# Optimization experiments

Hardware: AMD Instinct MI355X
Metric: run time of the kernel (lower is better)

## Reference

```python
import jax, jax.numpy as jnp
import numpy as np

EPS = 1e-5
STD = 0.02  # BERT initializer_range


def _bn(x, g, b):
    # BatchNorm1d in training mode: batch stats, biased variance
    m = jnp.mean(x, axis=0)
    v = jnp.mean((x - m) ** 2, axis=0)
    return g * (x - m) / jnp.sqrt(v + EPS) + b


def _gcn(x, src, dst, deg_isqrt, W, b, N):
    norm = deg_isqrt[src] * deg_isqrt[dst]
    msg = (x @ W)[src] * norm[:, None]
    return jax.ops.segment_sum(msg, dst, num_segments=N) + b


def setup_inputs() -> dict:
    key = jax.random.key(0)
    ks = jax.random.split(key, 24)
    B, S, E = 64, 512, 768
    D = E // 2            # 384, embed_size_gnn
    NG = 512              # nodes per graph
    N = B * NG            # 32768 total nodes
    Edges = 1048576
    C = 3                 # num_classes

    inp = {}
    inp["last_h"] = jax.random.normal(ks[0], (B, S, E), jnp.float32)
    inp["first_h"] = jax.random.normal(ks[1], (B, S, E), jnp.float32)
    inp["x_nodes"] = jax.random.normal(ks[2], (N, 300), jnp.float32)
    inp["edge_index"] = jax.random.randint(ks[3], (2, Edges), 0, N, jnp.int32)

    # exactly 2 masked nodes per sample (model reshapes to [B, 2, D])
    rng = np.random.default_rng(0)
    mask = np.zeros((B, NG), np.int32)
    for i in range(B):
        pos = rng.choice(NG, size=2, replace=False)
        mask[i, pos] = 1
    inp["graph_masking"] = jnp.asarray(mask)

    # params (stored [in, out]; torch Linear is [out, in])
    inp["w_pre1"] = STD * jax.random.normal(ks[4], (300, D), jnp.float32)
    inp["b_pre1"] = jnp.zeros((D,), jnp.float32)
    inp["w_pre2"] = STD * jax.random.normal(ks[5], (D, D), jnp.float32)
    inp["b_pre2"] = jnp.zeros((D,), jnp.float32)
    inp["w_conv"] = STD * jax.random.normal(ks[6], (3, D, D), jnp.float32)
    inp["b_conv"] = jnp.zeros((3, D), jnp.float32)
    inp["bng_g"] = jnp.ones((7, D), jnp.float32)
    inp["bng_b"] = jnp.zeros((7, D), jnp.float32)
    inp["w_post1"] = STD * jax.random.normal(ks[7], (D, D), jnp.float32)
    inp["b_post1"] = jnp.zeros((D,), jnp.float32)
    inp["w_post2"] = STD * jax.random.normal(ks[8], (D, D), jnp.float32)
    inp["b_post2"] = jnp.zeros((D,), jnp.float32)
    inp["w_cat"] = STD * jax.random.normal(ks[9], (E, E), jnp.float32)
    inp["b_cat"] = jnp.zeros((E,), jnp.float32)
    inp["bn_g"] = jnp.ones((2, E), jnp.float32)
    inp["bn_b"] = jnp.zeros((2, E), jnp.float32)
    inp["w_out"] = STD * jax.random.normal(ks[10], (E, C), jnp.float32)
    inp["b_out"] = jnp.zeros((C,), jnp.float32)
    return inp


def reference(last_h, first_h, x_nodes, edge_index, graph_masking,
              w_pre1, b_pre1, w_pre2, b_pre2, w_conv, b_conv, bng_g, bng_b,
              w_post1, b_post1, w_post2, b_post2, w_cat, b_cat, bn_g, bn_b,
              w_out, b_out):
    relu = jax.nn.relu
    B, NG = graph_masking.shape
    N = x_nodes.shape[0]

    # sentence branch: first/last hidden-state average, mean pool
    H_sent = jnp.mean(0.5 * (last_h + first_h), axis=1)  # [B, E]

    # GNN pre-MLPs
    x = _bn(relu(x_nodes @ w_pre1 + b_pre1), bng_g[0], bng_b[0])
    x = _bn(relu(x @ w_pre2 + b_pre2), bng_g[1], bng_b[1])

    # self-loop-augmented edge list, degree norm (shared across convs)
    loop = jnp.arange(N, dtype=edge_index.dtype)
    src = jnp.concatenate([edge_index[0], loop])
    dst = jnp.concatenate([edge_index[1], loop])
    deg = jax.ops.segment_sum(jnp.ones_like(dst, jnp.float32), dst, num_segments=N)
    deg_isqrt = jax.lax.rsqrt(deg)

    out = x
    for i in range(3):
        out = _bn(relu(_gcn(x, src, dst, deg_isqrt, w_conv[i], b_conv[i], N)),
                  bng_g[i + 2], bng_b[i + 2])

    out = _bn(relu(out @ w_post1 + b_post1), bng_g[5], bng_b[5])
    out = _bn(relu(out @ w_post2 + b_post2), bng_g[6], bng_b[6])  # [N, D]

    # reshape_graph_embeddings: gather the 2 masked nodes per sample
    # nodes are laid out contiguously per graph (NG nodes each)
    _, sel = jax.lax.top_k(graph_masking, 2)           # [B, 2] local idx, ascending on ties
    gidx = jnp.arange(B)[:, None] * NG + sel            # global node idx
    nodes = out[gidx]                                   # [B, 2, D]
    flat = nodes.reshape(B, -1)                         # [B, E]

    outc = _bn(relu(flat @ w_cat + b_cat), bn_g[0], bn_b[0])
    att = _bn(H_sent, bn_g[1], bn_b[1]) + outc
    return att @ w_out + b_out                          # [B, num_classes]
```

## Files before the change

### kernel.cpp

```cpp
#include <hip/hip_runtime.h>

typedef unsigned int uint32;
typedef unsigned short ushort16;

typedef __attribute__((ext_vector_type(8))) short bf16x8;
typedef __attribute__((ext_vector_type(4))) float f32x4;

#define NNODES 32768
#define DFEAT 384
#define KPAD1 320

__device__ __forceinline__ float bf2f(ushort16 u) {
  union { uint32 i; float f; } x; x.i = ((uint32)u) << 16; return x.f;
}
__device__ __forceinline__ float bflo(uint32 v) {
  union { uint32 i; float f; } x; x.i = v << 16; return x.f;
}
__device__ __forceinline__ float bfhi(uint32 v) {
  union { uint32 i; float f; } x; x.i = v & 0xffff0000u; return x.f;
}
__device__ __forceinline__ ushort16 f2bf(float f) {
  union { float f; uint32 i; } x; x.f = f;
  uint32 r = (x.i + 0x7fffu + ((x.i >> 16) & 1u)) >> 16;
  return (ushort16)r;
}

__global__ void convert_x_kernel(const float* __restrict__ X, ushort16* __restrict__ A0) {
  int row = blockIdx.x * 4 + (threadIdx.x >> 6);
  int lane = threadIdx.x & 63;
  const float* xr = X + (size_t)row * 300;
  ushort16* ar = A0 + (size_t)row * KPAD1;
#pragma unroll
  for (int i = 0; i < 5; ++i) {
    int col = lane + i * 64;
    float v = (col < 300) ? xr[col] : 0.f;
    ar[col] = f2bf(v);
  }
}

__global__ void sent_mean_kernel(const float* __restrict__ last,
                                 const float* __restrict__ first,
                                 float* __restrict__ Hpart) {
  int b = blockIdx.x, sc = blockIdx.y, e = threadIdx.x;
  int s0 = sc * 32;
  const float* pl = last + ((size_t)b * 512 + s0) * 768 + e;
  const float* pf = first + ((size_t)b * 512 + s0) * 768 + e;
  float a0 = 0.f, a1 = 0.f, a2 = 0.f, a3 = 0.f;
  for (int i = 0; i < 32; i += 4) {
    a0 += pl[(i + 0) * 768] + pf[(i + 0) * 768];
    a1 += pl[(i + 1) * 768] + pf[(i + 1) * 768];
    a2 += pl[(i + 2) * 768] + pf[(i + 2) * 768];
    a3 += pl[(i + 3) * 768] + pf[(i + 3) * 768];
  }
  Hpart[((size_t)sc * 64 + b) * 768 + e] = a0 + a1 + a2 + a3;
}
__global__ void hsent_kernel(const float* __restrict__ Hpart, float* __restrict__ Hsent) {
  int b = blockIdx.x, e = threadIdx.x;
  float h = 0.f;
#pragma unroll
  for (int sc = 0; sc < 16; ++sc) h += Hpart[((size_t)sc * 64 + b) * 768 + e];
  Hsent[(size_t)b * 768 + e] = h * (0.5f / 512.f);
}

__global__ void deg_count_kernel(const int* __restrict__ dst, int* __restrict__ cnt, int E) {
  int e = blockIdx.x * blockDim.x + threadIdx.x;
  if (e < E) atomicAdd(&cnt[dst[e]], 1);
}
__global__ void disq_kernel(const int* __restrict__ cnt, float* __restrict__ disq) {
  int n = blockIdx.x * blockDim.x + threadIdx.x;
  if (n < NNODES) disq[n] = rsqrtf((float)cnt[n] + 1.0f);
}
__global__ void scan_kernel(const int* __restrict__ cnt, int* __restrict__ row_start,
                            int* __restrict__ cursor) {
  __shared__ int buf[1024];
  int t = threadIdx.x;
  int base = t * 32;
  int s = 0;
  for (int i = 0; i < 32; ++i) s += cnt[base + i];
  buf[t] = s; __syncthreads();
  int x = s;
  for (int off = 1; off < 1024; off <<= 1) {
    int v = (t >= off) ? buf[t - off] : 0;
    __syncthreads();
    x += v; buf[t] = x;
    __syncthreads();
  }
  int run = x - s;
  for (int i = 0; i < 32; ++i) {
    row_start[base + i] = run; cursor[base + i] = run;
    run += cnt[base + i];
  }
  if (t == 1023) row_start[NNODES] = run;
}
__global__ void scatter_kernel(const int* __restrict__ src, const int* __restrict__ dst,
                               int* __restrict__ cursor, int* __restrict__ csr, int E) {
  int e = blockIdx.x * blockDim.x + threadIdx.x;
  if (e < E) {
    int d = dst[e];
    int pos = atomicAdd(&cursor[d], 1);
    csr[pos] = src[e];
  }
}

__global__ void xform_w_kernel(const float* __restrict__ W, const float* __restrict__ bias,
                               const float* __restrict__ stat, const float* __restrict__ g,
                               const float* __restrict__ bb, float invN,
                               ushort16* __restrict__ BT, float* __restrict__ bias_out,
                               int K, int Kpad, int Nw) {
  __shared__ float red[128];
  int n = blockIdx.x, t = threadIdx.x;
  float part = 0.f;
  for (int k = t; k < Kpad; k += 128) {
    ushort16 o = 0; float contrib = 0.f;
    if (k < K) {
      float ak = 1.f, shk = 0.f;
      if (stat) {
        float s = 0.f, q = 0.f;
        for (int i = 0; i < 8; ++i) { s += stat[k * 8 + i]; q += stat[(DFEAT + k) * 8 + i]; }
        float mean = s * invN, var = q * invN - mean * mean;
        ak = g[k] * rsqrtf(var + 1e-5f);
        shk = bb[k] - ak * mean;
      }
      float w = W[(size_t)k * Nw + n];
      o = f2bf(ak * w);
      contrib = shk * w;
    }
    BT[(size_t)n * Kpad + k] = o;
    part += contrib;
  }
  red[t] = part; __syncthreads();
  for (int off = 64; off > 0; off >>= 1) {
    if (t < off) red[t] += red[t + off];
    __syncthreads();
  }
  if (t == 0) bias_out[n] = (bias ? bias[n] : 0.f) + red[0];
}

#define BM 128
#define BN 128
#define BKT 32
#define LDT 40

template <bool RELU, bool STATS, bool RSCALE>
__global__ __launch_bounds__(256) void gemm_bf16(
    const ushort16* __restrict__ A, int lda, const ushort16* __restrict__ BT, int ldb,
    const float* __restrict__ bias, const float* __restrict__ rowscale,
    ushort16* __restrict__ C, int Ntot, int K, float* __restrict__ stat) {
  __shared__ __attribute__((aligned(16))) ushort16 As[BM * LDT];
  __shared__ __attribute__((aligned(16))) ushort16 Bs[BN * LDT];
  __shared__ float ssum[BN], ssq[BN];
  int bm0 = blockIdx.x * BM, bn0 = blockIdx.y * BN;
  int tid = threadIdx.x;
  if (STATS) {
    if (tid < BN) { ssum[tid] = 0.f; ssq[tid] = 0.f; }
  }
  int lane = tid & 63, wave = tid >> 6;
  int wm = (wave & 1) * 64, wn = (wave >> 1) * 64;
  int l15 = lane & 15, quad = lane >> 4;

  f32x4 acc[4][4];
  for (int i = 0; i < 4; ++i)
    for (int j = 0; j < 4; ++j) acc[i][j] = (f32x4)0.f;

  for (int kk = 0; kk < K; kk += BKT) {
    __syncthreads();
    for (int i = 0; i < 2; ++i) {
      int chunk = tid + i * 256;
      int row = chunk >> 2, cc = chunk & 3;
      uint4 va = *(const uint4*)(A + (size_t)(bm0 + row) * lda + kk + cc * 8);
      *(uint4*)(&As[row * LDT + cc * 8]) = va;
      uint4 vb = *(const uint4*)(BT + (size_t)(bn0 + row) * ldb + kk + cc * 8);
      *(uint4*)(&Bs[row * LDT + cc * 8]) = vb;
    }
    __syncthreads();
    bf16x8 af[4], bfr[4];
    for (int mi = 0; mi < 4; ++mi)
      af[mi] = *(const bf16x8*)(&As[(wm + mi * 16 + l15) * LDT + quad * 8]);
    for (int ni = 0; ni < 4; ++ni)
      bfr[ni] = *(const bf16x8*)(&Bs[(wn + ni * 16 + l15) * LDT + quad * 8]);
    for (int mi = 0; mi < 4; ++mi)
      for (int ni = 0; ni < 4; ++ni)
        acc[mi][ni] = __builtin_amdgcn_mfma_f32_16x16x32_bf16(af[mi], bfr[ni], acc[mi][ni], 0, 0, 0);
  }
  for (int ni = 0; ni < 4; ++ni) {
    int coll = wn + ni * 16 + l15;
    int col = bn0 + coll;
    float bv = bias[col];
    float s = 0.f, q = 0.f;
    for (int mi = 0; mi < 4; ++mi) {
      for (int r = 0; r < 4; ++r) {
        int row = bm0 + wm + mi * 16 + quad * 4 + r;
        float v = acc[mi][ni][r] + bv;
        if (RELU) v = fmaxf(v, 0.f);
        if (RSCALE) v *= rowscale[row];
        C[(size_t)row * Ntot + col] = f2bf(v);
        if (STATS) { s += v; q += v * v; }
      }
    }
    if (STATS) { atomicAdd(&ssum[coll], s); atomicAdd(&ssq[coll], q); }
  }
  if (STATS) {
    __syncthreads();
    int sp = blockIdx.x & 7;
    if (tid < BN) {
      atomicAdd(&stat[(bn0 + tid) * 8 + sp], ssum[tid]);
      atomicAdd(&stat[(DFEAT + bn0 + tid) * 8 + sp], ssq[tid]);
    }
  }
}

__global__ void __launch_bounds__(256) aggregate_kernel(
    const uint32* __restrict__ XWs, const int* __restrict__ csr,
    const int* __restrict__ row_start, const float* __restrict__ disq,
    const float* __restrict__ bconv, uint32* __restrict__ RC2,
    float* __restrict__ stat) {
  int bx = blockIdx.x;
  int slot = bx & 7, g = bx >> 3;
  int chunk = slot < 6 ? slot : (slot == 6 ? 0 : 3);
  int noff = slot < 6 ? 0 : 16384;
  int ngrp = (slot == 0 || slot == 3 || slot >= 6) ? 512 : 1024;
  if (g >= ngrp) return;
  __shared__ float ssum[64], ssq[64];
  int tid = threadIdx.x;
  if (tid < 64) { ssum[tid] = 0.f; ssq[tid] = 0.f; }
  __syncthreads();
  int lane = tid & 63, wave = tid >> 6;
  int half = lane >> 5, cl = lane & 31;
  int hb = half << 5;
  int cbase = chunk * 32;
  float b0 = bconv[chunk * 64 + 2 * cl], b1 = bconv[chunk * 64 + 2 * cl + 1];
  float ls0 = 0.f, ls1 = 0.f, lq0 = 0.f, lq1 = 0.f;
  int nodebase = noff + (g * 4 + wave) * 8;
  for (int ni = 0; ni < 8; ++ni) {
    int n = nodebase + ni;
    int beg = row_start[n], end = row_start[n + 1];
    int deg = end - beg;
    int len0 = (deg + 1) >> 1;
    int myBeg = beg + (half ? len0 : 0);
    int myLen = half ? (deg - len0) : len0;
    float a0, a1;
    if (half == 0) {
      uint32 v = XWs[(size_t)n * 192 + cbase + cl];
      a0 = bflo(v); a1 = bfhi(v);
    } else { a0 = 0.f; a1 = 0.f; }
    for (int bb0 = 0; bb0 < len0; bb0 += 32) {
      int rem = myLen - bb0;
      int idx = (cl < rem) ? csr[myBeg + bb0 + cl] : -1;
      int jmax = min(32, len0 - bb0);
      int j = 0;
      for (; j + 8 <= jmax; j += 8) {
        uint32 v[8];
#pragma unroll
        for (int jj = 0; jj < 8; ++jj) {
          int s = __shfl(idx, hb + j + jj, 64);
          int sa = (s < 0) ? 0 : s;
          uint32 m = (s < 0) ? 0u : 0xffffffffu;
          v[jj] = XWs[(size_t)sa * 192 + cbase + cl] & m;
        }
#pragma unroll
        for (int jj = 0; jj < 8; ++jj) { a0 += bflo(v[jj]); a1 += bfhi(v[jj]); }
      }
      for (; j < jmax; ++j) {
        int s = __shfl(idx, hb + j, 64);
        int sa = (s < 0) ? 0 : s;
        uint32 m = (s < 0) ? 0u : 0xffffffffu;
        uint32 v = XWs[(size_t)sa * 192 + cbase + cl] & m;
        a0 += bflo(v); a1 += bfhi(v);
      }
    }
    a0 += __shfl_xor(a0, 32, 64);
    a1 += __shfl_xor(a1, 32, 64);
    if (half == 0) {
      float din = disq[n];
      a0 = fmaxf(din * a0 + b0, 0.f);
      a1 = fmaxf(din * a1 + b1, 0.f);
      RC2[(size_t)n * 192 + cbase + cl] = (uint32)f2bf(a0) | ((uint32)f2bf(a1) << 16);
      ls0 += a0; lq0 += a0 * a0; ls1 += a1; lq1 += a1 * a1;
    }
  }
  if (half == 0) {
    atomicAdd(&ssum[2 * cl], ls0); atomicAdd(&ssum[2 * cl + 1], ls1);
    atomicAdd(&ssq[2 * cl], lq0);  atomicAdd(&ssq[2 * cl + 1], lq1);
  }
  __syncthreads();
  if (tid < 64) {
    int col = chunk * 64 + tid;
    int sp = g & 7;
    atomicAdd(&stat[col * 8 + sp], ssum[tid]);
    atomicAdd(&stat[(DFEAT + col) * 8 + sp], ssq[tid]);
  }
}

__global__ void gather_kernel(const int* __restrict__ mask, const ushort16* __restrict__ R5,
                              const float* __restrict__ stat, const float* __restrict__ g,
                              const float* __restrict__ bb, float invN,
                              float* __restrict__ flat) {
  __shared__ int smin, smax;
  int b = blockIdx.x, t = threadIdx.x;
  if (t == 0) { smin = 1 << 30; smax = -1; }
  __syncthreads();
  for (int p = t; p < 512; p += 384)
    if (mask[b * 512 + p]) { atomicMin(&smin, p); atomicMax(&smax, p); }
  __syncthreads();
  float s = 0.f, q = 0.f;
  for (int i = 0; i < 8; ++i) { s += stat[t * 8 + i]; q += stat[(DFEAT + t) * 8 + i]; }
  float mean = s * invN, var = q * invN - mean * mean;
  float a = g[t] * rsqrtf(var + 1e-5f), sh = bb[t] - a * mean;
  int sel[2] = {smin, smax};
  for (int j = 0; j < 2; ++j) {
    float v = bf2f(R5[(size_t)(b * 512 + sel[j]) * DFEAT + t]);
    flat[(size_t)b * 768 + j * DFEAT + t] = a * v + sh;
  }
}

__global__ void cat_gemm_kernel(const float* __restrict__ flat, const float* __restrict__ Wc,
                                const float* __restrict__ bc, float* __restrict__ out) {
  int t = threadIdx.x;
  int j = blockIdx.x * 64 + (t & 63);
  int b = blockIdx.y * 16 + (t >> 6);
  const float* fr = flat + (size_t)b * 768;
  float acc = bc[j];
#pragma unroll 4
  for (int k = 0; k < 768; ++k) acc += fr[k] * Wc[(size_t)k * 768 + j];
  out[(size_t)b * 768 + j] = fmaxf(acc, 0.f);
}
__global__ void bnstats_kernel(const float* __restrict__ catrelu, const float* __restrict__ Hsent,
                               const float* __restrict__ g, const float* __restrict__ bb,
                               float* __restrict__ aff) {
  int c = blockIdx.x * 64 + threadIdx.x;
  float s1 = 0, q1 = 0, s2 = 0, q2 = 0;
  for (int b = 0; b < 64; ++b) {
    float v = catrelu[b * 768 + c]; s1 += v; q1 += v * v;
    float h = Hsent[b * 768 + c];   s2 += h; q2 += h * h;
  }
  const float inv = 1.0f / 64.0f;
  float m1 = s1 * inv, var1 = q1 * inv - m1 * m1;
  float a1 = g[c] * rsqrtf(var1 + 1e-5f);
  aff[c] = a1; aff[768 + c] = bb[c] - a1 * m1;
  float m2 = s2 * inv, var2 = q2 * inv - m2 * m2;
  float a2 = g[768 + c] * rsqrtf(var2 + 1e-5f);
  aff[1536 + c] = a2; aff[2304 + c] = bb[768 + c] - a2 * m2;
}
__global__ void final_kernel(const float* __restrict__ Hs, const float* __restrict__ catrelu,
                             const float* __restrict__ aff, const float* __restrict__ w_out,
                             const float* __restrict__ b_out, float* __restrict__ out) {
  __shared__ float red[12];
  int b = blockIdx.x, t = threadIdx.x;
  float p0 = 0, p1 = 0, p2 = 0;
  for (int k = t; k < 768; k += 256) {
    float att = (aff[1536 + k] * Hs[b * 768 + k] + aff[2304 + k]) +
                (aff[k] * catrelu[b * 768 + k] + aff[768 + k]);
    p0 += att * w_out[k * 3 + 0];
    p1 += att * w_out[k * 3 + 1];
    p2 += att * w_out[k * 3 + 2];
  }
  for (int off = 32; off > 0; off >>= 1) {
    p0 += __shfl_down(p0, off, 64);
    p1 += __shfl_down(p1, off, 64);
    p2 += __shfl_down(p2, off, 64);
  }
  int wv = t >> 6;
  if ((t & 63) == 0) { red[wv * 3 + 0] = p0; red[wv * 3 + 1] = p1; red[wv * 3 + 2] = p2; }
  __syncthreads();
  if (t == 0) {
    out[b * 3 + 0] = b_out[0] + red[0] + red[3] + red[6] + red[9];
    out[b * 3 + 1] = b_out[1] + red[1] + red[4] + red[7] + red[10];
    out[b * 3 + 2] = b_out[2] + red[2] + red[5] + red[8] + red[11];
  }
}

extern "C" void kernel_launch(void* const* d_in, const int* in_sizes, int n_in,
                              void* d_out, int out_size, void* d_ws, size_t ws_size,
                              hipStream_t stream) {
  const float* last_h  = (const float*)d_in[0];
  const float* first_h = (const float*)d_in[1];
  const float* x_nodes = (const float*)d_in[2];
  const int*   edges   = (const int*)d_in[3];
  const int*   mask    = (const int*)d_in[4];
  const float* w_pre1  = (const float*)d_in[5];
  const float* b_pre1  = (const float*)d_in[6];
  const float* w_pre2  = (const float*)d_in[7];
  const float* b_pre2  = (const float*)d_in[8];
  const float* w_conv  = (const float*)d_in[9];
  const float* b_conv  = (const float*)d_in[10];
  const float* bng_g   = (const float*)d_in[11];
  const float* bng_b   = (const float*)d_in[12];
  const float* w_post1 = (const float*)d_in[13];
  const float* b_post1 = (const float*)d_in[14];
  const float* w_post2 = (const float*)d_in[15];
  const float* b_post2 = (const float*)d_in[16];
  const float* w_cat   = (const float*)d_in[17];
  const float* b_cat   = (const float*)d_in[18];
  const float* bn_g    = (const float*)d_in[19];
  const float* bn_b    = (const float*)d_in[20];
  const float* w_out   = (const float*)d_in[21];
  const float* b_out   = (const float*)d_in[22];
  float* out = (float*)d_out;

  const int E = in_sizes[3] / 2;
  const int* e_src = edges;
  const int* e_dst = edges + E;

  char* w = (char*)d_ws;
  size_t off = 0;
  auto alloc = [&](size_t bytes) { size_t p = off; off = (off + bytes + 255) & ~(size_t)255; return p; };
  ushort16* buf0   = (ushort16*)(w + alloc((size_t)NNODES * DFEAT * 2));
  ushort16* buf1   = (ushort16*)(w + alloc((size_t)NNODES * DFEAT * 2));
  int*    csr      = (int*)(w + alloc((size_t)E * 4));
  int*    rowstart = (int*)(w + alloc((size_t)(NNODES + 1) * 4));
  int*    cursor   = (int*)(w + alloc((size_t)NNODES * 4));
  float*  disq     = (float*)(w + alloc((size_t)NNODES * 4));
  ushort16* BT     = (ushort16*)(w + alloc((size_t)DFEAT * DFEAT * 2));
  float*  biasx    = (float*)(w + alloc(DFEAT * 4));
  float*  flat     = (float*)(w + alloc(64 * 768 * 4));
  float*  catrelu  = (float*)(w + alloc(64 * 768 * 4));
  float*  aff64    = (float*)(w + alloc(4 * 768 * 4));
  float*  Hpart    = (float*)(w + alloc((size_t)16 * 64 * 768 * 4));
  float*  Hsent    = (float*)(w + alloc(64 * 768 * 4));
  size_t zoff = off;
  int*   degcnt = (int*)(w + alloc((size_t)NNODES * 4));
  float* stats  = (float*)(w + alloc((size_t)5 * 768 * 8 * 4));
  size_t zbytes = off - zoff;

  hipMemsetAsync(w + zoff, 0, zbytes, stream);

  const float invN = 1.0f / (float)NNODES;
  float* st0 = stats + 0 * 768 * 8;
  float* st1 = stats + 1 * 768 * 8;
  float* st2 = stats + 2 * 768 * 8;
  float* st3 = stats + 3 * 768 * 8;
  float* st4 = stats + 4 * 768 * 8;

  convert_x_kernel<<<NNODES / 4, 256, 0, stream>>>(x_nodes, buf0);
  xform_w_kernel<<<DFEAT, 128, 0, stream>>>(w_pre1, b_pre1, nullptr, nullptr, nullptr, invN, BT, biasx, 300, KPAD1, DFEAT);
  sent_mean_kernel<<<dim3(64, 16), 768, 0, stream>>>(last_h, first_h, Hpart);
  hsent_kernel<<<64, 768, 0, stream>>>(Hpart, Hsent);
  deg_count_kernel<<<(E + 255) / 256, 256, 0, stream>>>(e_dst, degcnt, E);
  disq_kernel<<<NNODES / 256, 256, 0, stream>>>(degcnt, disq);
  scan_kernel<<<1, 1024, 0, stream>>>(degcnt, rowstart, cursor);
  scatter_kernel<<<(E + 255) / 256, 256, 0, stream>>>(e_src, e_dst, cursor, csr, E);

  dim3 ggrid(NNODES / BM, DFEAT / BN);

  gemm_bf16<true, true, false><<<ggrid, 256, 0, stream>>>(buf0, KPAD1, BT, KPAD1, biasx, nullptr, buf1, DFEAT, KPAD1, st0);
  xform_w_kernel<<<DFEAT, 128, 0, stream>>>(w_pre2, b_pre2, st0, bng_g + 0 * DFEAT, bng_b + 0 * DFEAT, invN, BT, biasx, DFEAT, DFEAT, DFEAT);

  gemm_bf16<true, true, false><<<ggrid, 256, 0, stream>>>(buf1, DFEAT, BT, DFEAT, biasx, nullptr, buf0, DFEAT, DFEAT, st1);
  xform_w_kernel<<<DFEAT, 128, 0, stream>>>(w_conv + 2 * DFEAT * DFEAT, nullptr, st1, bng_g + 1 * DFEAT, bng_b + 1 * DFEAT, invN, BT, biasx, DFEAT, DFEAT, DFEAT);

  gemm_bf16<false, false, true><<<ggrid, 256, 0, stream>>>(buf0, DFEAT, BT, DFEAT, biasx, disq, buf1, DFEAT, DFEAT, nullptr);

  aggregate_kernel<<<8192, 256, 0, stream>>>((const uint32*)buf1, csr, rowstart, disq, b_conv + 2 * DFEAT, (uint32*)buf0, st2);
  xform_w_kernel<<<DFEAT, 128, 0, stream>>>(w_post1, b_post1, st2, bng_g + 4 * DFEAT, bng_b + 4 * DFEAT, invN, BT, biasx, DFEAT, DFEAT, DFEAT);

  gemm_bf16<true, true, false><<<ggrid, 256, 0, stream>>>(buf0, DFEAT, BT, DFEAT, biasx, nullptr, buf1, DFEAT, DFEAT, st3);
  xform_w_kernel<<<DFEAT, 128, 0, stream>>>(w_post2, b_post2, st3, bng_g + 5 * DFEAT, bng_b + 5 * DFEAT, invN, BT, biasx, DFEAT, DFEAT, DFEAT);

  gemm_bf16<true, true, false><<<ggrid, 256, 0, stream>>>(buf1, DFEAT, BT, DFEAT, biasx, nullptr, buf0, DFEAT, DFEAT, st4);

  gather_kernel<<<64, DFEAT, 0, stream>>>(mask, buf0, st4, bng_g + 6 * DFEAT, bng_b + 6 * DFEAT, invN, flat);
  cat_gemm_kernel<<<dim3(12, 4), 1024, 0, stream>>>(flat, w_cat, b_cat, catrelu);
  bnstats_kernel<<<12, 64, 0, stream>>>(catrelu, Hsent, bn_g, bn_b, aff64);
  final_kernel<<<64, 256, 0, stream>>>(Hsent, catrelu, aff64, w_out, b_out, out);
}
```

Baseline: 905.2 us.

## Fuse preprocessing kernels and widen aggregate gathers to 8-byte loads

Merges the x conversion, degree counting and sentence-mean partial sums into one horizontally fused launch. The rsqrt degree normalisation moves into the scan kernel, and the Hsent reduction is folded into the scatter kernel, which cuts the number of small launches and lets independent work overlap. The aggregate kernel now has each lane load 4 bf16 features (uint2) and splits each half-wave into two 16-lane subgroups that process alternating edges, with an unmasked fast path and a cross-lane reduction at the end. This adds block-index branching and more complex tail handling in exchange for fewer launches and wider gather loads.

```diff
diff --git a/kernel.cpp b/kernel.cpp
--- a/kernel.cpp
+++ b/kernel.cpp
@@ -25,58 +25,56 @@
   return (ushort16)r;
 }
 
-__global__ void convert_x_kernel(const float* __restrict__ X, ushort16* __restrict__ A0) {
-  int row = blockIdx.x * 4 + (threadIdx.x >> 6);
-  int lane = threadIdx.x & 63;
-  const float* xr = X + (size_t)row * 300;
-  ushort16* ar = A0 + (size_t)row * KPAD1;
+__global__ __launch_bounds__(256) void prep_kernel(
+    const float* __restrict__ X, ushort16* __restrict__ A0,
+    const int* __restrict__ dst, int* __restrict__ cnt, int E, int degB,
+    const float* __restrict__ last, const float* __restrict__ first,
+    float* __restrict__ Hpart) {
+  int bx = blockIdx.x;
+  int tid = threadIdx.x;
+  if (bx < 8192) {
+    int row = bx * 4 + (tid >> 6);
+    int lane = tid & 63;
+    const float* xr = X + (size_t)row * 300;
+    ushort16* ar = A0 + (size_t)row * KPAD1;
 #pragma unroll
-  for (int i = 0; i < 5; ++i) {
-    int col = lane + i * 64;
-    float v = (col < 300) ? xr[col] : 0.f;
-    ar[col] = f2bf(v);
-  }
-}
-
-__global__ void sent_mean_kernel(const float* __restrict__ last,
-                                 const float* __restrict__ first,
-                                 float* __restrict__ Hpart) {
-  int b = blockIdx.x, sc = blockIdx.y, e = threadIdx.x;
-  int s0 = sc * 32;
-  const float* pl = last + ((size_t)b * 512 + s0) * 768 + e;
-  const float* pf = first + ((size_t)b * 512 + s0) * 768 + e;
-  float a0 = 0.f, a1 = 0.f, a2 = 0.f, a3 = 0.f;
-  for (int i = 0; i < 32; i += 4) {
-    a0 += pl[(i + 0) * 768] + pf[(i + 0) * 768];
-    a1 += pl[(i + 1) * 768] + pf[(i + 1) * 768];
-    a2 += pl[(i + 2) * 768] + pf[(i + 2) * 768];
-    a3 += pl[(i + 3) * 768] + pf[(i + 3) * 768];
-  }
-  Hpart[((size_t)sc * 64 + b) * 768 + e] = a0 + a1 + a2 + a3;
-}
-__global__ void hsent_kernel(const float* __restrict__ Hpart, float* __restrict__ Hsent) {
-  int b = blockIdx.x, e = threadIdx.x;
-  float h = 0.f;
-#pragma unroll
-  for (int sc = 0; sc < 16; ++sc) h += Hpart[((size_t)sc * 64 + b) * 768 + e];
-  Hsent[(size_t)b * 768 + e] = h * (0.5f / 512.f);
-}
-
-__global__ void deg_count_kernel(const int* __restrict__ dst, int* __restrict__ cnt, int E) {
-  int e = blockIdx.x * blockDim.x + threadIdx.x;
-  if (e < E) atomicAdd(&cnt[dst[e]], 1);
-}
-__global__ void disq_kernel(const int* __restrict__ cnt, float* __restrict__ disq) {
-  int n = blockIdx.x * blockDim.x + threadIdx.x;
-  if (n < NNODES) disq[n] = rsqrtf((float)cnt[n] + 1.0f);
-}
+    for (int i = 0; i < 5; ++i) {
+      int col = lane + i * 64;
+      float v = (col < 300) ? xr[col] : 0.f;
+      ar[col] = f2bf(v);
+    }
+  } else if (bx < 8192 + degB) {
+    int e = (bx - 8192) * 256 + tid;
+    if (e < E) atomicAdd(&cnt[dst[e]], 1);
+  } else {
+    int idx = bx - 8192 - degB;
+    int b = idx & 63, sc = (idx >> 6) & 15, es = idx >> 10;
+    int e = es * 256 + tid;
+    int s0 = sc * 32;
+    const float* pl = last + ((size_t)b * 512 + s0) * 768 + e;
+    const float* pf = first + ((size_t)b * 512 + s0) * 768 + e;
+    float a0 = 0.f, a1 = 0.f, a2 = 0.f, a3 = 0.f;
+    for (int i = 0; i < 32; i += 4) {
+      a0 += pl[(i + 0) * 768] + pf[(i + 0) * 768];
+      a1 += pl[(i + 1) * 768] + pf[(i + 1) * 768];
+      a2 += pl[(i + 2) * 768] + pf[(i + 2) * 768];
+      a3 += pl[(i + 3) * 768] + pf[(i + 3) * 768];
+    }
+    Hpart[((size_t)sc * 64 + b) * 768 + e] = a0 + a1 + a2 + a3;
+  }
+}
+
 __global__ void scan_kernel(const int* __restrict__ cnt, int* __restrict__ row_start,
-                            int* __restrict__ cursor) {
+                            int* __restrict__ cursor, float* __restrict__ disq) {
   __shared__ int buf[1024];
   int t = threadIdx.x;
   int base = t * 32;
   int s = 0;
-  for (int i = 0; i < 32; ++i) s += cnt[base + i];
+  for (int i = 0; i < 32; ++i) {
+    int c = cnt[base + i];
+    s += c;
+    disq[base + i] = rsqrtf((float)c + 1.0f);
+  }
   buf[t] = s; __syncthreads();
   int x = s;
   for (int off = 1; off < 1024; off <<= 1) {
@@ -92,13 +90,27 @@
   }
   if (t == 1023) row_start[NNODES] = run;
 }
-__global__ void scatter_kernel(const int* __restrict__ src, const int* __restrict__ dst,
-                               int* __restrict__ cursor, int* __restrict__ csr, int E) {
-  int e = blockIdx.x * blockDim.x + threadIdx.x;
-  if (e < E) {
-    int d = dst[e];
-    int pos = atomicAdd(&cursor[d], 1);
-    csr[pos] = src[e];
+
+__global__ __launch_bounds__(256) void scatter_kernel(
+    const int* __restrict__ src, const int* __restrict__ dst,
+    int* __restrict__ cursor, int* __restrict__ csr, int E, int degB,
+    const float* __restrict__ Hpart, float* __restrict__ Hsent) {
+  int bx = blockIdx.x, t = threadIdx.x;
+  if (bx < degB) {
+    int e = bx * 256 + t;
+    if (e < E) {
+      int d = dst[e];
+      int pos = atomicAdd(&cursor[d], 1);
+      csr[pos] = src[e];
+    }
+  } else {
+    int idx = bx - degB;
+    int b = idx & 63, es = idx >> 6;
+    int e = es * 256 + t;
+    float h = 0.f;
+#pragma unroll
+    for (int sc = 0; sc < 16; ++sc) h += Hpart[((size_t)sc * 64 + b) * 768 + e];
+    Hsent[(size_t)b * 768 + e] = h * (0.5f / 512.f);
   }
 }
 
@@ -225,11 +237,17 @@
   if (tid < 64) { ssum[tid] = 0.f; ssq[tid] = 0.f; }
   __syncthreads();
   int lane = tid & 63, wave = tid >> 6;
-  int half = lane >> 5, cl = lane & 31;
+  int half = lane >> 5;
+  int sub = (lane >> 4) & 1;
+  int ll = lane & 15;
+  int cl = lane & 31;
   int hb = half << 5;
-  int cbase = chunk * 32;
-  float b0 = bconv[chunk * 64 + 2 * cl], b1 = bconv[chunk * 64 + 2 * cl + 1];
-  float ls0 = 0.f, ls1 = 0.f, lq0 = 0.f, lq1 = 0.f;
+  int hsub = hb + sub;
+  const uint2* XW2 = (const uint2*)XWs;
+  int coff = chunk * 16 + ll;
+  float4 bq = *(const float4*)(bconv + chunk * 64 + 4 * ll);
+  float ls0 = 0.f, ls1 = 0.f, ls2 = 0.f, ls3 = 0.f;
+  float lq0 = 0.f, lq1 = 0.f, lq2 = 0.f, lq3 = 0.f;
   int nodebase = noff + (g * 4 + wave) * 8;
   for (int ni = 0; ni < 8; ++ni) {
     int n = nodebase + ni;
@@ -238,49 +256,70 @@
     int len0 = (deg + 1) >> 1;
     int myBeg = beg + (half ? len0 : 0);
     int myLen = half ? (deg - len0) : len0;
-    float a0, a1;
-    if (half == 0) {
-      uint32 v = XWs[(size_t)n * 192 + cbase + cl];
-      a0 = bflo(v); a1 = bfhi(v);
-    } else { a0 = 0.f; a1 = 0.f; }
+    float a0, a1, a2, a3;
+    if (lane < 16) {
+      uint2 v = XW2[(size_t)n * 96 + coff];
+      a0 = bflo(v.x); a1 = bfhi(v.x); a2 = bflo(v.y); a3 = bfhi(v.y);
+    } else { a0 = 0.f; a1 = 0.f; a2 = 0.f; a3 = 0.f; }
     for (int bb0 = 0; bb0 < len0; bb0 += 32) {
       int rem = myLen - bb0;
       int idx = (cl < rem) ? csr[myBeg + bb0 + cl] : -1;
       int jmax = min(32, len0 - bb0);
-      int j = 0;
-      for (; j + 8 <= jmax; j += 8) {
-        uint32 v[8];
+      int remMin = (deg - len0) - bb0;
+      int nfast = min(jmax, max(remMin, 0)) & ~1;
+      int jj = 0;
+      for (; jj + 16 <= nfast; jj += 16) {
+        uint2 v[8];
 #pragma unroll
-        for (int jj = 0; jj < 8; ++jj) {
-          int s = __shfl(idx, hb + j + jj, 64);
-          int sa = (s < 0) ? 0 : s;
-          uint32 m = (s < 0) ? 0u : 0xffffffffu;
-          v[jj] = XWs[(size_t)sa * 192 + cbase + cl] & m;
+        for (int u = 0; u < 8; ++u) {
+          int s = __shfl(idx, hsub + jj + 2 * u, 64);
+          v[u] = XW2[(size_t)s * 96 + coff];
         }
 #pragma unroll
-        for (int jj = 0; jj < 8; ++jj) { a0 += bflo(v[jj]); a1 += bfhi(v[jj]); }
+        for (int u = 0; u < 8; ++u) {
+          a0 += bflo(v[u].x); a1 += bfhi(v[u].x);
+          a2 += bflo(v[u].y); a3 += bfhi(v[u].y);
+        }
       }
-      for (; j < jmax; ++j) {
-        int s = __shfl(idx, hb + j, 64);
-        int sa = (s < 0) ? 0 : s;
-        uint32 m = (s < 0) ? 0u : 0xffffffffu;
-        uint32 v = XWs[(size_t)sa * 192 + cbase + cl] & m;
-        a0 += bflo(v); a1 += bfhi(v);
+      for (; jj + 2 <= nfast; jj += 2) {
+        int s = __shfl(idx, hsub + jj, 64);
+        uint2 v = XW2[(size_t)s * 96 + coff];
+        a0 += bflo(v.x); a1 += bfhi(v.x); a2 += bflo(v.y); a3 += bfhi(v.y);
       }
-    }
-    a0 += __shfl_xor(a0, 32, 64);
-    a1 += __shfl_xor(a1, 32, 64);
-    if (half == 0) {
+      for (; jj < jmax; jj += 2) {
+        int e0 = jj + sub;
+        int s = __shfl(idx, hb + (e0 & 31), 64);
+        bool val = (e0 < jmax) && (s >= 0);
+        int sa = val ? s : 0;
+        uint32 m = val ? 0xffffffffu : 0u;
+        uint2 v = XW2[(size_t)sa * 96 + coff];
+        v.x &= m; v.y &= m;
+        a0 += bflo(v.x); a1 += bfhi(v.x); a2 += bflo(v.y); a3 += bfhi(v.y);
+      }
+    }
+    a0 += __shfl_xor(a0, 16, 64); a1 += __shfl_xor(a1, 16, 64);
+    a2 += __shfl_xor(a2, 16, 64); a3 += __shfl_xor(a3, 16, 64);
+    a0 += __shfl_xor(a0, 32, 64); a1 += __shfl_xor(a1, 32, 64);
+    a2 += __shfl_xor(a2, 32, 64); a3 += __shfl_xor(a3, 32, 64);
+    if (lane < 16) {
       float din = disq[n];
-      a0 = fmaxf(din * a0 + b0, 0.f);
-      a1 = fmaxf(din * a1 + b1, 0.f);
-      RC2[(size_t)n * 192 + cbase + cl] = (uint32)f2bf(a0) | ((uint32)f2bf(a1) << 16);
+      a0 = fmaxf(din * a0 + bq.x, 0.f);
+      a1 = fmaxf(din * a1 + bq.y, 0.f);
+      a2 = fmaxf(din * a2 + bq.z, 0.f);
+      a3 = fmaxf(din * a3 + bq.w, 0.f);
+      uint2 o;
+      o.x = (uint32)f2bf(a0) | ((uint32)f2bf(a1) << 16);
+      o.y = (uint32)f2bf(a2) | ((uint32)f2bf(a3) << 16);
+      *(uint2*)&RC2[(size_t)n * 192 + chunk * 32 + 2 * ll] = o;
       ls0 += a0; lq0 += a0 * a0; ls1 += a1; lq1 += a1 * a1;
-    }
-  }
-  if (half == 0) {
-    atomicAdd(&ssum[2 * cl], ls0); atomicAdd(&ssum[2 * cl + 1], ls1);
-    atomicAdd(&ssq[2 * cl], lq0);  atomicAdd(&ssq[2 * cl + 1], lq1);
+      ls2 += a2; lq2 += a2 * a2; ls3 += a3; lq3 += a3 * a3;
+    }
+  }
+  if (lane < 16) {
+    atomicAdd(&ssum[4 * ll + 0], ls0); atomicAdd(&ssq[4 * ll + 0], lq0);
+    atomicAdd(&ssum[4 * ll + 1], ls1); atomicAdd(&ssq[4 * ll + 1], lq1);
+    atomicAdd(&ssum[4 * ll + 2], ls2); atomicAdd(&ssq[4 * ll + 2], lq2);
+    atomicAdd(&ssum[4 * ll + 3], ls3); atomicAdd(&ssq[4 * ll + 3], lq3);
   }
   __syncthreads();
   if (tid < 64) {
@@ -400,6 +439,7 @@
   const int E = in_sizes[3] / 2;
   const int* e_src = edges;
   const int* e_dst = edges + E;
+  const int degB = (E + 255) / 256;
 
   char* w = (char*)d_ws;
   size_t off = 0;
@@ -431,14 +471,11 @@
   float* st3 = stats + 3 * 768 * 8;
   float* st4 = stats + 4 * 768 * 8;
 
-  convert_x_kernel<<<NNODES / 4, 256, 0, stream>>>(x_nodes, buf0);
+  prep_kernel<<<8192 + degB + 3072, 256, 0, stream>>>(x_nodes, buf0, e_dst, degcnt, E, degB,
+                                                      last_h, first_h, Hpart);
   xform_w_kernel<<<DFEAT, 128, 0, stream>>>(w_pre1, b_pre1, nullptr, nullptr, nullptr, invN, BT, biasx, 300, KPAD1, DFEAT);
-  sent_mean_kernel<<<dim3(64, 16), 768, 0, stream>>>(last_h, first_h, Hpart);
-  hsent_kernel<<<64, 768, 0, stream>>>(Hpart, Hsent);
-  deg_count_kernel<<<(E + 255) / 256, 256, 0, stream>>>(e_dst, degcnt, E);
-  disq_kernel<<<NNODES / 256, 256, 0, stream>>>(degcnt, disq);
-  scan_kernel<<<1, 1024, 0, stream>>>(degcnt, rowstart, cursor);
-  scatter_kernel<<<(E + 255) / 256, 256, 0, stream>>>(e_src, e_dst, cursor, csr, E);
+  scan_kernel<<<1, 1024, 0, stream>>>(degcnt, rowstart, cursor, disq);
+  scatter_kernel<<<degB + 192, 256, 0, stream>>>(e_src, e_dst, cursor, csr, E, degB, Hpart, Hsent);
 
   dim3 ggrid(NNODES / BM, DFEAT / BN);
 
```

After: 946.8 us. 1.05x slower.

## Fuse preprocessing kernels into shared launches and compact aggregate grid mapping

Applied to the files above, without the earlier changes.

Merges the x conversion, degree counting and sentence-sum partials into one heterogeneous prep kernel. It folds the rsqrt degree computation into the scan and the Hsent reduction into the scatter launch, cutting the launch count. The aggregate kernel's block-to-(chunk, node group) mapping is replaced by a dense 6144-block layout, so the 2048 blocks that exited immediately are no longer launched. Independent work now overlaps inside each launch, at the cost of mixed block types and possible load imbalance.

```diff
diff --git a/kernel.cpp b/kernel.cpp
--- a/kernel.cpp
+++ b/kernel.cpp
@@ -25,58 +25,56 @@
   return (ushort16)r;
 }
 
-__global__ void convert_x_kernel(const float* __restrict__ X, ushort16* __restrict__ A0) {
-  int row = blockIdx.x * 4 + (threadIdx.x >> 6);
-  int lane = threadIdx.x & 63;
-  const float* xr = X + (size_t)row * 300;
-  ushort16* ar = A0 + (size_t)row * KPAD1;
+__global__ __launch_bounds__(256) void prep_kernel(
+    const float* __restrict__ X, ushort16* __restrict__ A0,
+    const int* __restrict__ dst, int* __restrict__ cnt, int E, int degB,
+    const float* __restrict__ last, const float* __restrict__ first,
+    float* __restrict__ Hpart) {
+  int bx = blockIdx.x;
+  int tid = threadIdx.x;
+  if (bx < 8192) {
+    int row = bx * 4 + (tid >> 6);
+    int lane = tid & 63;
+    const float* xr = X + (size_t)row * 300;
+    ushort16* ar = A0 + (size_t)row * KPAD1;
 #pragma unroll
-  for (int i = 0; i < 5; ++i) {
-    int col = lane + i * 64;
-    float v = (col < 300) ? xr[col] : 0.f;
-    ar[col] = f2bf(v);
-  }
-}
-
-__global__ void sent_mean_kernel(const float* __restrict__ last,
-                                 const float* __restrict__ first,
-                                 float* __restrict__ Hpart) {
-  int b = blockIdx.x, sc = blockIdx.y, e = threadIdx.x;
-  int s0 = sc * 32;
-  const float* pl = last + ((size_t)b * 512 + s0) * 768 + e;
-  const float* pf = first + ((size_t)b * 512 + s0) * 768 + e;
-  float a0 = 0.f, a1 = 0.f, a2 = 0.f, a3 = 0.f;
-  for (int i = 0; i < 32; i += 4) {
-    a0 += pl[(i + 0) * 768] + pf[(i + 0) * 768];
-    a1 += pl[(i + 1) * 768] + pf[(i + 1) * 768];
-    a2 += pl[(i + 2) * 768] + pf[(i + 2) * 768];
-    a3 += pl[(i + 3) * 768] + pf[(i + 3) * 768];
-  }
-  Hpart[((size_t)sc * 64 + b) * 768 + e] = a0 + a1 + a2 + a3;
-}
-__global__ void hsent_kernel(const float* __restrict__ Hpart, float* __restrict__ Hsent) {
-  int b = blockIdx.x, e = threadIdx.x;
-  float h = 0.f;
-#pragma unroll
-  for (int sc = 0; sc < 16; ++sc) h += Hpart[((size_t)sc * 64 + b) * 768 + e];
-  Hsent[(size_t)b * 768 + e] = h * (0.5f / 512.f);
-}
-
-__global__ void deg_count_kernel(const int* __restrict__ dst, int* __restrict__ cnt, int E) {
-  int e = blockIdx.x * blockDim.x + threadIdx.x;
-  if (e < E) atomicAdd(&cnt[dst[e]], 1);
-}
-__global__ void disq_kernel(const int* __restrict__ cnt, float* __restrict__ disq) {
-  int n = blockIdx.x * blockDim.x + threadIdx.x;
-  if (n < NNODES) disq[n] = rsqrtf((float)cnt[n] + 1.0f);
-}
+    for (int i = 0; i < 5; ++i) {
+      int col = lane + i * 64;
+      float v = (col < 300) ? xr[col] : 0.f;
+      ar[col] = f2bf(v);
+    }
+  } else if (bx < 8192 + degB) {
+    int e = (bx - 8192) * 256 + tid;
+    if (e < E) atomicAdd(&cnt[dst[e]], 1);
+  } else {
+    int idx = bx - 8192 - degB;
+    int b = idx & 63, sc = (idx >> 6) & 15, es = idx >> 10;
+    int e = es * 256 + tid;
+    int s0 = sc * 32;
+    const float* pl = last + ((size_t)b * 512 + s0) * 768 + e;
+    const float* pf = first + ((size_t)b * 512 + s0) * 768 + e;
+    float a0 = 0.f, a1 = 0.f, a2 = 0.f, a3 = 0.f;
+    for (int i = 0; i < 32; i += 4) {
+      a0 += pl[(i + 0) * 768] + pf[(i + 0) * 768];
+      a1 += pl[(i + 1) * 768] + pf[(i + 1) * 768];
+      a2 += pl[(i + 2) * 768] + pf[(i + 2) * 768];
+      a3 += pl[(i + 3) * 768] + pf[(i + 3) * 768];
+    }
+    Hpart[((size_t)sc * 64 + b) * 768 + e] = a0 + a1 + a2 + a3;
+  }
+}
+
 __global__ void scan_kernel(const int* __restrict__ cnt, int* __restrict__ row_start,
-                            int* __restrict__ cursor) {
+                            int* __restrict__ cursor, float* __restrict__ disq) {
   __shared__ int buf[1024];
   int t = threadIdx.x;
   int base = t * 32;
   int s = 0;
-  for (int i = 0; i < 32; ++i) s += cnt[base + i];
+  for (int i = 0; i < 32; ++i) {
+    int c = cnt[base + i];
+    s += c;
+    disq[base + i] = rsqrtf((float)c + 1.0f);
+  }
   buf[t] = s; __syncthreads();
   int x = s;
   for (int off = 1; off < 1024; off <<= 1) {
@@ -92,13 +90,27 @@
   }
   if (t == 1023) row_start[NNODES] = run;
 }
-__global__ void scatter_kernel(const int* __restrict__ src, const int* __restrict__ dst,
-                               int* __restrict__ cursor, int* __restrict__ csr, int E) {
-  int e = blockIdx.x * blockDim.x + threadIdx.x;
-  if (e < E) {
-    int d = dst[e];
-    int pos = atomicAdd(&cursor[d], 1);
-    csr[pos] = src[e];
+
+__global__ __launch_bounds__(256) void scatter_kernel(
+    const int* __restrict__ src, const int* __restrict__ dst,
+    int* __restrict__ cursor, int* __restrict__ csr, int E, int degB,
+    const float* __restrict__ Hpart, float* __restrict__ Hsent) {
+  int bx = blockIdx.x, t = threadIdx.x;
+  if (bx < degB) {
+    int e = bx * 256 + t;
+    if (e < E) {
+      int d = dst[e];
+      int pos = atomicAdd(&cursor[d], 1);
+      csr[pos] = src[e];
+    }
+  } else {
+    int idx = bx - degB;
+    int b = idx & 63, es = idx >> 6;
+    int e = es * 256 + t;
+    float h = 0.f;
+#pragma unroll
+    for (int sc = 0; sc < 16; ++sc) h += Hpart[((size_t)sc * 64 + b) * 768 + e];
+    Hsent[(size_t)b * 768 + e] = h * (0.5f / 512.f);
   }
 }
 
@@ -215,11 +227,9 @@
     const float* __restrict__ bconv, uint32* __restrict__ RC2,
     float* __restrict__ stat) {
   int bx = blockIdx.x;
-  int slot = bx & 7, g = bx >> 3;
-  int chunk = slot < 6 ? slot : (slot == 6 ? 0 : 3);
-  int noff = slot < 6 ? 0 : 16384;
-  int ngrp = (slot == 0 || slot == 3 || slot >= 6) ? 512 : 1024;
-  if (g >= ngrp) return;
+  int unit = (bx & 7) * 768 + (bx >> 3);
+  int chunk = unit >> 10;
+  int g = unit & 1023;
   __shared__ float ssum[64], ssq[64];
   int tid = threadIdx.x;
   if (tid < 64) { ssum[tid] = 0.f; ssq[tid] = 0.f; }
@@ -230,7 +240,7 @@
   int cbase = chunk * 32;
   float b0 = bconv[chunk * 64 + 2 * cl], b1 = bconv[chunk * 64 + 2 * cl + 1];
   float ls0 = 0.f, ls1 = 0.f, lq0 = 0.f, lq1 = 0.f;
-  int nodebase = noff + (g * 4 + wave) * 8;
+  int nodebase = (g * 4 + wave) * 8;
   for (int ni = 0; ni < 8; ++ni) {
     int n = nodebase + ni;
     int beg = row_start[n], end = row_start[n + 1];
@@ -400,6 +410,7 @@
   const int E = in_sizes[3] / 2;
   const int* e_src = edges;
   const int* e_dst = edges + E;
+  const int degB = (E + 255) / 256;
 
   char* w = (char*)d_ws;
   size_t off = 0;
@@ -431,14 +442,11 @@
   float* st3 = stats + 3 * 768 * 8;
   float* st4 = stats + 4 * 768 * 8;
 
-  convert_x_kernel<<<NNODES / 4, 256, 0, stream>>>(x_nodes, buf0);
+  prep_kernel<<<8192 + degB + 3072, 256, 0, stream>>>(x_nodes, buf0, e_dst, degcnt, E, degB,
+                                                      last_h, first_h, Hpart);
   xform_w_kernel<<<DFEAT, 128, 0, stream>>>(w_pre1, b_pre1, nullptr, nullptr, nullptr, invN, BT, biasx, 300, KPAD1, DFEAT);
-  sent_mean_kernel<<<dim3(64, 16), 768, 0, stream>>>(last_h, first_h, Hpart);
-  hsent_kernel<<<64, 768, 0, stream>>>(Hpart, Hsent);
-  deg_count_kernel<<<(E + 255) / 256, 256, 0, stream>>>(e_dst, degcnt, E);
-  disq_kernel<<<NNODES / 256, 256, 0, stream>>>(degcnt, disq);
-  scan_kernel<<<1, 1024, 0, stream>>>(degcnt, rowstart, cursor);
-  scatter_kernel<<<(E + 255) / 256, 256, 0, stream>>>(e_src, e_dst, cursor, csr, E);
+  scan_kernel<<<1, 1024, 0, stream>>>(degcnt, rowstart, cursor, disq);
+  scatter_kernel<<<degB + 192, 256, 0, stream>>>(e_src, e_dst, cursor, csr, E, degB, Hpart, Hsent);
 
   dim3 ggrid(NNODES / BM, DFEAT / BN);
 
@@ -450,7 +458,7 @@
 
   gemm_bf16<false, false, true><<<ggrid, 256, 0, stream>>>(buf0, DFEAT, BT, DFEAT, biasx, disq, buf1, DFEAT, DFEAT, nullptr);
 
-  aggregate_kernel<<<8192, 256, 0, stream>>>((const uint32*)buf1, csr, rowstart, disq, b_conv + 2 * DFEAT, (uint32*)buf0, st2);
+  aggregate_kernel<<<6144, 256, 0, stream>>>((const uint32*)buf1, csr, rowstart, disq, b_conv + 2 * DFEAT, (uint32*)buf0, st2);
   xform_w_kernel<<<DFEAT, 128, 0, stream>>>(w_post1, b_post1, st2, bng_g + 4 * DFEAT, bng_b + 4 * DFEAT, invN, BT, biasx, DFEAT, DFEAT, DFEAT);
 
   gemm_bf16<true, true, false><<<ggrid, 256, 0, stream>>>(buf0, DFEAT, BT, DFEAT, biasx, nullptr, buf1, DFEAT, DFEAT, st3);
```

Result: faster. 853.2 us (-5.7%).
